# Kernel optimization log

Hardware: AMD Instinct MI355X
Metric: run time of the kernel (lower is better)

Reference implementation:

```python
import jax, jax.numpy as jnp
import numpy as np

H = 4  # attention heads for the single degree-0 fiber

def _layer_norm(x, gamma):
    mu = x.mean(-1, keepdims=True)
    var = ((x - mu) ** 2).mean(-1, keepdims=True)
    return (x - mu) / jnp.sqrt(var + 1e-5) * gamma

def _silu(x):
    return x * jax.nn.sigmoid(x)

def _forward(features, rel_dist, norm_scale, Wq, Wxi, Wxj,
             rp_W1, rp_b1, rp_g1, rp_W2, rp_b2, rp_g2, rp_W3, rp_b3,
             Wkv_out, Wout, neighbor_indices, neighbor_mask):
    b, n, d, _ = features.shape
    k = neighbor_indices.shape[-1]
    hid = Wq.shape[1]
    dh = hid // H
    kvd = Wkv_out.shape[0]
    scale = dh ** -0.5

    # ---- prenorm: RMS (over feature channels) of per-m L2 norms; m=1 for degree 0
    rms = jnp.sqrt(jnp.sum(features ** 2, axis=-2, keepdims=True)) * (d ** -0.5)
    x = features / jnp.maximum(rms, 1e-12) * norm_scale      # (b,n,d,1)
    x = x[..., 0]                                            # (b,n,d)

    # ---- queries
    q = x @ Wq                                               # (b,n,hid)

    # ---- DTP to_kv (degree0->degree0): project xi/xj, gather neighbors, radial kernel
    xi = x @ Wxi
    xj = x @ Wxj
    xg = jax.vmap(lambda t, idx: t[idx])(xj, neighbor_indices)   # (b,n,k,d)
    xe = xg + xi[:, :, None, :]

    hdd = _layer_norm(_silu(rel_dist @ rp_W1 + rp_b1), rp_g1)    # (b,n,k,rh)
    hdd = _layer_norm(_silu(hdd @ rp_W2 + rp_b2), rp_g2)
    R = (hdd @ rp_W3 + rp_b3).reshape(b, n, k, kvd, d)           # per-edge (lo,li) kernel
    kv = jnp.einsum('bnkod,bnkd->bnko', R, xe)                   # (b,n,k,kvd)
    kv = kv @ Wkv_out                                            # DTP project_out
    kk, vv = jnp.split(kv, 2, axis=-1)                           # (b,n,k,hid) each

    # ---- L2-distance attention over neighbors
    qh = q.reshape(b, n, H, dh).transpose(0, 2, 1, 3)            # (b,h,n,dh)
    kh = kk.reshape(b, n, k, H, dh).transpose(0, 3, 1, 2, 4)     # (b,h,n,k,dh)
    vh = vv.reshape(b, n, k, H, dh).transpose(0, 3, 1, 2, 4)
    diff = qh[:, :, :, None, :] - kh + 1e-6                      # F.pairwise_distance eps
    sim = -jnp.sqrt(jnp.sum(diff * diff, axis=-1)) * scale       # (b,h,n,k)
    sim = jnp.where(neighbor_mask[:, None], sim, -jnp.finfo(sim.dtype).max)
    attn = jax.nn.softmax(sim, axis=-1)
    out = jnp.einsum('bhnk,bhnkd->bhnd', attn, vh)
    out = out.transpose(0, 2, 1, 3).reshape(b, n, hid)

    return (out @ Wout)[..., None]                               # (b,n,d,1)

def setup_inputs() -> dict:
    key = jax.random.key(0)
    ks = jax.random.split(key, 16)
    b, n, k, d = 2, 256, 16, 64
    hid = H * 32           # heads * dim_head = 128
    kvd = 2 * hid          # 256
    rh = 64                # radial_hidden_dim
    rnd = lambda i, shape, s=1.0: jax.random.normal(ks[i], shape, jnp.float32) * s
    return dict(
        features=rnd(0, (b, n, d, 1)),
        neighbor_indices=jax.random.randint(ks[1], (b, n, k), 0, n),
        neighbor_mask=jax.random.bernoulli(ks[2], 0.9, (b, n, k)),
        rel_dist=jax.random.uniform(ks[3], (b, n, k, 1), jnp.float32),
        norm_scale=jnp.ones((d, 1), jnp.float32),
        Wq=rnd(4, (d, hid), d ** -0.5),
        Wxi=rnd(5, (d, d), d ** -0.5),
        Wxj=rnd(6, (d, d), d ** -0.5),
        rp_W1=rnd(7, (1, rh)), rp_b1=jnp.zeros((rh,), jnp.float32),
        rp_g1=jnp.ones((rh,), jnp.float32),
        rp_W2=rnd(8, (rh, rh), rh ** -0.5), rp_b2=jnp.zeros((rh,), jnp.float32),
        rp_g2=jnp.ones((rh,), jnp.float32),
        rp_W3=rnd(9, (rh, kvd * d), rh ** -0.5), rp_b3=jnp.zeros((kvd * d,), jnp.float32),
        Wkv_out=rnd(10, (kvd, kvd), kvd ** -0.5),
        Wout=rnd(11, (hid, d), hid ** -0.5),
    )

def reference(features, neighbor_indices, neighbor_mask, rel_dist, norm_scale,
              Wq, Wxi, Wxj, rp_W1, rp_b1, rp_g1, rp_W2, rp_b2, rp_g2,
              rp_W3, rp_b3, Wkv_out, Wout):
    return _forward(features, rel_dist, norm_scale, Wq, Wxi, Wxj,
                    rp_W1, rp_b1, rp_g1, rp_W2, rp_b2, rp_g2, rp_W3, rp_b3,
                    Wkv_out, Wout, neighbor_indices, neighbor_mask)
```

## Files before the change

kernel.cpp:

```cpp
#include <hip/hip_runtime.h>
#include <hip/hip_bf16.h>
#include <float.h>

#define BB 2
#define NN 256
#define DD 64
#define KK 16
#define NH 4
#define HID 128
#define KVD 256
#define RH 64
#define NNODES (BB*NN)
#define NEDGES (NNODES*KK)

typedef unsigned int uint32;
typedef unsigned short ushort_t;
typedef float f32x4_t __attribute__((ext_vector_type(4)));
typedef short bf16x8_t __attribute__((ext_vector_type(8)));
typedef __attribute__((address_space(3))) ushort_t lds_us;
typedef __attribute__((address_space(1))) const ushort_t glb_us;

__device__ __forceinline__ uint32 cvtpk_bf16(float lo, float hi) {
  uint32 r;
  asm("v_cvt_pk_bf16_f32 %0, %1, %2" : "=v"(r) : "v"(lo), "v"(hi));
  return r;
}

__device__ __forceinline__ float wave_sum64(float v) {
  #pragma unroll
  for (int m = 32; m; m >>= 1) v += __shfl_xor(v, m, 64);
  return v;
}

__device__ __forceinline__ ushort_t rne_bf16(float f) {
  uint32 u = __float_as_uint(f);
  return (ushort_t)((u + 0x7FFFu + ((u >> 16) & 1u)) >> 16);
}

__global__ __launch_bounds__(256) void node_w3_kernel(
    const float* __restrict__ feat, const float* __restrict__ gscale,
    const float* __restrict__ Wq, const float* __restrict__ Wxi,
    const float* __restrict__ Wxj,
    const float* __restrict__ W3, const float* __restrict__ b3,
    const float* __restrict__ Wkv,
    float* __restrict__ q_ws, float* __restrict__ xi_ws, float* __restrict__ xj_ws,
    ushort_t* __restrict__ W3bf, ushort_t* __restrict__ Wkvt) {
  int bx = blockIdx.x;
  if (bx >= 648) {
    int i = ((bx - 648) * 256 + threadIdx.x) * 4;
    int n = i >> 8, k0 = i & 255;
    union { uint2 q; ushort_t s[4]; } o;
    #pragma unroll
    for (int j = 0; j < 4; ++j) o.s[j] = rne_bf16(Wkv[(k0 + j) * KVD + n]);
    *(uint2*)(Wkvt + n * KVD + k0) = o.q;
    return;
  }
  if (bx >= 128) {
    const int W3N = 64 * KVD * DD;
    int i = ((bx - 128) * 256 + threadIdx.x) * 8;
    const float* src = (i < W3N) ? (W3 + i) : (b3 + (i - W3N));
    float4 a = ((const float4*)src)[0];
    float4 b = ((const float4*)src)[1];
    float v[8] = {a.x, a.y, a.z, a.w, b.x, b.y, b.z, b.w};
    union { uint4 q; ushort_t s[8]; } o;
    #pragma unroll
    for (int jj = 0; jj < 8; ++jj) o.s[jj] = rne_bf16(v[jj]);
    int rr = i >> 14, j0 = i & 16383;
    int oc = j0 >> 6, gr = (j0 >> 3) & 7;
    int byte_sw = oc * 128 + ((gr * 16) ^ ((oc & 7) << 4));
    *(uint4*)(W3bf + (rr << 14) + (byte_sw >> 1)) = o.q;
    return;
  }
  int sub = threadIdx.x >> 6;
  int t = threadIdx.x & 63;
  int node = bx * 4 + sub;
  __shared__ float xs[4][DD];
  float f = feat[node * DD + t];
  float ss = wave_sum64(f * f);
  float rms = sqrtf(ss) * 0.125f;
  float den = fmaxf(rms, 1e-12f);
  float x = f / den * gscale[t];
  xs[sub][t] = x;
  __syncthreads();
  float q0 = 0.f, q1 = 0.f, xiv = 0.f, xjv = 0.f;
  #pragma unroll 4
  for (int d = 0; d < DD; ++d) {
    float xv = xs[sub][d];
    q0  += xv * Wq[d * HID + t];
    q1  += xv * Wq[d * HID + 64 + t];
    xiv += xv * Wxi[d * DD + t];
    xjv += xv * Wxj[d * DD + t];
  }
  q_ws[node * HID + t] = q0;
  q_ws[node * HID + 64 + t] = q1;
  xi_ws[node * DD + t] = xiv;
  xj_ws[node * DD + t] = xjv;
}

#define AFRAG(dst, arr, base, h) {                                \
  union { bf16x8_t v; uint32 u[4]; } t_;                          \
  t_.u[0] = cvtpk_bf16(arr[(base)+0]*(h), arr[(base)+1]*(h));     \
  t_.u[1] = cvtpk_bf16(arr[(base)+2]*(h), arr[(base)+3]*(h));     \
  t_.u[2] = cvtpk_bf16(arr[(base)+4]*(h), arr[(base)+5]*(h));     \
  t_.u[3] = cvtpk_bf16(arr[(base)+6]*(h), arr[(base)+7]*(h));     \
  dst = t_.v; }

#define STAGE2(buf, rr) {                                                      \
  const ushort_t* s_ = W3bf + ((size_t)(rr) << 14);                            \
  ushort_t* d_ = &bstage[buf][0];                                              \
  __builtin_amdgcn_global_load_lds((glb_us*)(s_ + tid * 8),         (lds_us*)(d_ + tid * 8),         16, 0, 0); \
  __builtin_amdgcn_global_load_lds((glb_us*)(s_ + 2048  + tid * 8), (lds_us*)(d_ + 2048  + tid * 8), 16, 0, 0); \
  __builtin_amdgcn_global_load_lds((glb_us*)(s_ + 4096  + tid * 8), (lds_us*)(d_ + 4096  + tid * 8), 16, 0, 0); \
  __builtin_amdgcn_global_load_lds((glb_us*)(s_ + 6144  + tid * 8), (lds_us*)(d_ + 6144  + tid * 8), 16, 0, 0); \
  __builtin_amdgcn_global_load_lds((glb_us*)(s_ + 8192  + tid * 8), (lds_us*)(d_ + 8192  + tid * 8), 16, 0, 0); \
  __builtin_amdgcn_global_load_lds((glb_us*)(s_ + 10240 + tid * 8), (lds_us*)(d_ + 10240 + tid * 8), 16, 0, 0); \
  __builtin_amdgcn_global_load_lds((glb_us*)(s_ + 12288 + tid * 8), (lds_us*)(d_ + 12288 + tid * 8), 16, 0, 0); \
  __builtin_amdgcn_global_load_lds((glb_us*)(s_ + 14336 + tid * 8), (lds_us*)(d_ + 14336 + tid * 8), 16, 0, 0); }

__global__ __launch_bounds__(256, 1) void fused_kernel(
    const int* __restrict__ nbi, const float* __restrict__ rel,
    const float* __restrict__ W1, const float* __restrict__ b1,
    const float* __restrict__ g1, const float* __restrict__ W2,
    const float* __restrict__ b2, const float* __restrict__ g2,
    const float* __restrict__ xi_ws, const float* __restrict__ xj_ws,
    const ushort_t* __restrict__ W3bf, const ushort_t* __restrict__ Wkvt,
    const float* __restrict__ q_ws, const int* __restrict__ maskp,
    const float* __restrict__ Wout, float* __restrict__ out) {
  int b = blockIdx.x;
  int tid = threadIdx.x;
  int wv = tid >> 6, l = tid & 63;
  int l15 = l & 15, g = l >> 4;

  __shared__ ushort_t bstage[2][16384];
  __shared__ float h2_s[32 * 68];
  __shared__ float xe_s[32 * 68];
  __shared__ float attn_s[2][NH * KK];
  __shared__ float o_s[2][HID];

  STAGE2(0, 0);

  {
    float w1r = W1[l], b1r = b1[l], g1r = g1[l];
    float b2r = b2[l], g2r = g2[l];
    float w2r[64];
    #pragma unroll
    for (int r = 0; r < 64; ++r) w2r[r] = W2[r * RH + l];
    int node_w = b * 2 + (wv >> 1);
    int bbn = node_w >> 8;
    float xir = xi_ws[node_w * DD + l];
    for (int i = 0; i < 8; ++i) {
      int e_loc = wv * 8 + i;
      float rd = rel[b * 32 + e_loc];
      float h = rd * w1r + b1r;
      h = h / (1.f + expf(-h));
      float mu = wave_sum64(h) * (1.f / RH);
      float c = h - mu;
      float var = wave_sum64(c * c) * (1.f / RH);
      float xn = c * rsqrtf(var + 1e-5f) * g1r;
      float p = b2r;
      #pragma unroll
      for (int r = 0; r < 64; ++r) {
        float s = __uint_as_float(__builtin_amdgcn_readlane(__float_as_uint(xn), r));
        p += s * w2r[r];
      }
      p = p / (1.f + expf(-p));
      mu = wave_sum64(p) * (1.f / RH);
      c = p - mu;
      var = wave_sum64(c * c) * (1.f / RH);
      float h2v = c * rsqrtf(var + 1e-5f) * g2r;
      h2_s[e_loc * 68 + l] = h2v;
      int nb = nbi[node_w * KK + (e_loc & 15)];
      xe_s[e_loc * 68 + l] = xj_ws[(bbn * NN + nb) * DD + l] + xir;
    }
  }
  asm volatile("s_waitcnt vmcnt(0)" ::: "memory");
  __syncthreads();

  float xfA[16], xfB[16];
  #pragma unroll
  for (int j = 0; j < 8; ++j) {
    xfA[j]     = xe_s[l15 * 68 + g * 8 + j];
    xfA[8 + j] = xe_s[l15 * 68 + 32 + g * 8 + j];
    xfB[j]     = xe_s[(16 + l15) * 68 + g * 8 + j];
    xfB[8 + j] = xe_s[(16 + l15) * 68 + 32 + g * 8 + j];
  }
  int swz = (l15 & 7) << 4;
  f32x4_t accA[4], accB[4];
  #pragma unroll
  for (int oi = 0; oi < 4; ++oi) {
    accA[oi] = (f32x4_t){0.f, 0.f, 0.f, 0.f};
    accB[oi] = (f32x4_t){0.f, 0.f, 0.f, 0.f};
  }
  int cur = 0;
  for (int p = 0; p <= 64; ++p) {
    if (p < 64) STAGE2(cur ^ 1, p + 1);
    float hA = (p < 64) ? h2_s[l15 * 68 + p] : 1.0f;
    float hB = (p < 64) ? h2_s[(16 + l15) * 68 + p] : 1.0f;
    bf16x8_t a0A, a1A, a0B, a1B;
    AFRAG(a0A, xfA, 0, hA); AFRAG(a1A, xfA, 8, hA);
    AFRAG(a0B, xfB, 0, hB); AFRAG(a1B, xfB, 8, hB);
    const char* bp = (const char*)&bstage[cur][0] + wv * 8192 + l15 * 128;
    #pragma unroll
    for (int oi = 0; oi < 4; ++oi) {
      bf16x8_t bv0 = *(const bf16x8_t*)(bp + oi * 2048 + ((g * 16) ^ swz));
      bf16x8_t bv1 = *(const bf16x8_t*)(bp + oi * 2048 + (((4 + g) * 16) ^ swz));
      accA[oi] = __builtin_amdgcn_mfma_f32_16x16x32_bf16(a0A, bv0, accA[oi], 0, 0, 0);
      accA[oi] = __builtin_amdgcn_mfma_f32_16x16x32_bf16(a1A, bv1, accA[oi], 0, 0, 0);
      accB[oi] = __builtin_amdgcn_mfma_f32_16x16x32_bf16(a0B, bv0, accB[oi], 0, 0, 0);
      accB[oi] = __builtin_amdgcn_mfma_f32_16x16x32_bf16(a1B, bv1, accB[oi], 0, 0, 0);
    }
    asm volatile("s_waitcnt vmcnt(0)" ::: "memory");
    __syncthreads();
    cur ^= 1;
  }

  float* kvf = (float*)&bstage[0][0];
  {
    #pragma unroll
    for (int m = 0; m < 2; ++m) {
      #pragma unroll
      for (int oi = 0; oi < 4; ++oi) {
        f32x4_t av = m ? accB[oi] : accA[oi];
        int f = wv * 64 + oi * 16 + l15;
        int fu = f >> 2, fl = f & 3;
        #pragma unroll
        for (int q = 0; q < 4; ++q) {
          int e = m * 16 + g * 4 + q;
          kvf[e * 256 + ((fu ^ (e & 7)) << 2) + fl] = av[q];
        }
      }
    }
  }
  __syncthreads();

  int role = wv & 1, nl = wv >> 1;
  int node = b * 2 + nl;
  bf16x8_t a[8];
  {
    int e = nl * 16 + l15;
    const float* kr = kvf + e * 256;
    int sw = l15 & 7;
    #pragma unroll
    for (int c = 0; c < 8; ++c) {
      int u0 = (c * 8 + g * 2) ^ sw;
      int u1 = (c * 8 + g * 2 + 1) ^ sw;
      f32x4_t v0 = *(const f32x4_t*)(kr + u0 * 4);
      f32x4_t v1 = *(const f32x4_t*)(kr + u1 * 4);
      union { bf16x8_t v; uint32 u[4]; } t_;
      t_.u[0] = cvtpk_bf16(v0.x, v0.y);
      t_.u[1] = cvtpk_bf16(v0.z, v0.w);
      t_.u[2] = cvtpk_bf16(v1.x, v1.y);
      t_.u[3] = cvtpk_bf16(v1.z, v1.w);
      a[c] = t_.v;
    }
  }
  f32x4_t acc[8];
  #pragma unroll
  for (int nt = 0; nt < 8; ++nt) {
    acc[nt] = (f32x4_t){0.f, 0.f, 0.f, 0.f};
    const ushort_t* bbase = Wkvt + (size_t)(role * 128 + nt * 16 + l15) * KVD + g * 8;
    #pragma unroll
    for (int c = 0; c < 8; ++c) {
      bf16x8_t bv = *(const bf16x8_t*)(bbase + c * 32);
      acc[nt] = __builtin_amdgcn_mfma_f32_16x16x32_bf16(a[c], bv, acc[nt], 0, 0, 0);
    }
  }
  const float scale = 0.17677669529663689f;
  if (role == 0) {
    float sim[4][4];
    #pragma unroll
    for (int h = 0; h < 4; ++h) {
      #pragma unroll
      for (int q = 0; q < 4; ++q) {
        float s = 0.f;
        #pragma unroll
        for (int pq = 0; pq < 2; ++pq) {
          int nt = h * 2 + pq;
          float qv = q_ws[node * HID + nt * 16 + l15];
          float diff = qv - acc[nt][q] + 1e-6f;
          s += diff * diff;
        }
        #pragma unroll
        for (int m = 8; m; m >>= 1) s += __shfl_xor(s, m, 64);
        sim[q][h] = -sqrtf(s) * scale;
      }
    }
    int mv[4];
    #pragma unroll
    for (int q = 0; q < 4; ++q) mv[q] = maskp[node * KK + g * 4 + q];
    #pragma unroll
    for (int h = 0; h < 4; ++h) {
      float sv[4];
      float mx = -FLT_MAX;
      #pragma unroll
      for (int q = 0; q < 4; ++q) {
        sv[q] = mv[q] ? sim[q][h] : -FLT_MAX;
        mx = fmaxf(mx, sv[q]);
      }
      mx = fmaxf(mx, __shfl_xor(mx, 16, 64));
      mx = fmaxf(mx, __shfl_xor(mx, 32, 64));
      float se = 0.f, ev[4];
      #pragma unroll
      for (int q = 0; q < 4; ++q) { ev[q] = expf(sv[q] - mx); se += ev[q]; }
      se += __shfl_xor(se, 16, 64);
      se += __shfl_xor(se, 32, 64);
      float inv = 1.f / se;
      if (l15 == 0) {
        #pragma unroll
        for (int q = 0; q < 4; ++q) attn_s[nl][h * KK + g * 4 + q] = ev[q] * inv;
      }
    }
  }
  __syncthreads();
  if (role == 1) {
    #pragma unroll
    for (int nt = 0; nt < 8; ++nt) {
      int h = nt >> 1;
      float o = 0.f;
      #pragma unroll
      for (int q = 0; q < 4; ++q) o += attn_s[nl][h * KK + g * 4 + q] * acc[nt][q];
      o += __shfl_xor(o, 16, 64);
      o += __shfl_xor(o, 32, 64);
      if (g == 0) o_s[nl][nt * 16 + l15] = o;
    }
  }
  __syncthreads();
  if (tid < 128) {
    int n2 = tid >> 6, t = tid & 63;
    float r = 0.f;
    #pragma unroll 4
    for (int cI = 0; cI < HID; ++cI) r += o_s[n2][cI] * Wout[cI * DD + t];
    out[(b * 2 + n2) * DD + t] = r;
  }
}

extern "C" void kernel_launch(void* const* d_in, const int* in_sizes, int n_in,
                              void* d_out, int out_size, void* d_ws, size_t ws_size,
                              hipStream_t stream) {
  const float* feat = (const float*)d_in[0];
  const int*   nbi  = (const int*)d_in[1];
  const int*   msk  = (const int*)d_in[2];
  const float* rel  = (const float*)d_in[3];
  const float* gsc  = (const float*)d_in[4];
  const float* Wq   = (const float*)d_in[5];
  const float* Wxi  = (const float*)d_in[6];
  const float* Wxj  = (const float*)d_in[7];
  const float* W1   = (const float*)d_in[8];
  const float* b1   = (const float*)d_in[9];
  const float* g1   = (const float*)d_in[10];
  const float* W2   = (const float*)d_in[11];
  const float* b2   = (const float*)d_in[12];
  const float* g2   = (const float*)d_in[13];
  const float* W3   = (const float*)d_in[14];
  const float* b3   = (const float*)d_in[15];
  const float* Wkv  = (const float*)d_in[16];
  const float* Wout = (const float*)d_in[17];

  float* ws      = (float*)d_ws;
  float* q_ws    = ws;
  float* xi_ws   = q_ws  + NNODES * HID;
  float* xj_ws   = xi_ws + NNODES * DD;
  ushort_t* W3bf = (ushort_t*)(xj_ws + NNODES * DD);
  ushort_t* Wkvt = W3bf + 65 * 16384;

  node_w3_kernel<<<712, 256, 0, stream>>>(feat, gsc, Wq, Wxi, Wxj, W3, b3, Wkv,
                                          q_ws, xi_ws, xj_ws, W3bf, Wkvt);
  fused_kernel<<<256, 256, 0, stream>>>(nbi, rel, W1, b1, g1, W2, b2, g2,
                                        xi_ws, xj_ws, W3bf, Wkvt,
                                        q_ws, msk, Wout, (float*)d_out);
}
```

Before: 189.9 us.

## Triple-buffer W3 staging with per-wave loads and drop per-iteration barriers

The W3 weight staging moves from a block-wide double buffer, synchronised by a barrier every iteration, to a triple buffer. Each wave now loads only its own 8 KB slice, so each wave reads only the LDS it fetched itself. The per-iteration s_waitcnt vmcnt(0) plus __syncthreads is replaced with counted vmcnt waits, which lets waves run ahead and keeps up to three stages of loads in flight. This costs an extra 32 KB of LDS and relies on exact vmcnt accounting. It also relies on the hA/hB reads from h2_s and the earlier global loads not disturbing those counts, which is fragile.

```diff
diff --git a/kernel.cpp b/kernel.cpp
--- a/kernel.cpp
+++ b/kernel.cpp
@@ -105,17 +105,17 @@
   t_.u[3] = cvtpk_bf16(arr[(base)+6]*(h), arr[(base)+7]*(h));     \
   dst = t_.v; }
 
-#define STAGE2(buf, rr) {                                                      \
-  const ushort_t* s_ = W3bf + ((size_t)(rr) << 14);                            \
-  ushort_t* d_ = &bstage[buf][0];                                              \
-  __builtin_amdgcn_global_load_lds((glb_us*)(s_ + tid * 8),         (lds_us*)(d_ + tid * 8),         16, 0, 0); \
-  __builtin_amdgcn_global_load_lds((glb_us*)(s_ + 2048  + tid * 8), (lds_us*)(d_ + 2048  + tid * 8), 16, 0, 0); \
-  __builtin_amdgcn_global_load_lds((glb_us*)(s_ + 4096  + tid * 8), (lds_us*)(d_ + 4096  + tid * 8), 16, 0, 0); \
-  __builtin_amdgcn_global_load_lds((glb_us*)(s_ + 6144  + tid * 8), (lds_us*)(d_ + 6144  + tid * 8), 16, 0, 0); \
-  __builtin_amdgcn_global_load_lds((glb_us*)(s_ + 8192  + tid * 8), (lds_us*)(d_ + 8192  + tid * 8), 16, 0, 0); \
-  __builtin_amdgcn_global_load_lds((glb_us*)(s_ + 10240 + tid * 8), (lds_us*)(d_ + 10240 + tid * 8), 16, 0, 0); \
-  __builtin_amdgcn_global_load_lds((glb_us*)(s_ + 12288 + tid * 8), (lds_us*)(d_ + 12288 + tid * 8), 16, 0, 0); \
-  __builtin_amdgcn_global_load_lds((glb_us*)(s_ + 14336 + tid * 8), (lds_us*)(d_ + 14336 + tid * 8), 16, 0, 0); }
+#define STAGEW(slot, rr) {                                                     \
+  const ushort_t* s_ = W3bf + ((size_t)(rr) << 14) + wv * 4096;                \
+  ushort_t* d_ = &bstage[slot][wv * 4096];                                     \
+  __builtin_amdgcn_global_load_lds((glb_us*)(s_ + l * 8),          (lds_us*)(d_ + l * 8),          16, 0, 0); \
+  __builtin_amdgcn_global_load_lds((glb_us*)(s_ + 512  + l * 8),   (lds_us*)(d_ + 512  + l * 8),   16, 0, 0); \
+  __builtin_amdgcn_global_load_lds((glb_us*)(s_ + 1024 + l * 8),   (lds_us*)(d_ + 1024 + l * 8),   16, 0, 0); \
+  __builtin_amdgcn_global_load_lds((glb_us*)(s_ + 1536 + l * 8),   (lds_us*)(d_ + 1536 + l * 8),   16, 0, 0); \
+  __builtin_amdgcn_global_load_lds((glb_us*)(s_ + 2048 + l * 8),   (lds_us*)(d_ + 2048 + l * 8),   16, 0, 0); \
+  __builtin_amdgcn_global_load_lds((glb_us*)(s_ + 2560 + l * 8),   (lds_us*)(d_ + 2560 + l * 8),   16, 0, 0); \
+  __builtin_amdgcn_global_load_lds((glb_us*)(s_ + 3072 + l * 8),   (lds_us*)(d_ + 3072 + l * 8),   16, 0, 0); \
+  __builtin_amdgcn_global_load_lds((glb_us*)(s_ + 3584 + l * 8),   (lds_us*)(d_ + 3584 + l * 8),   16, 0, 0); }
 
 __global__ __launch_bounds__(256, 1) void fused_kernel(
     const int* __restrict__ nbi, const float* __restrict__ rel,
@@ -131,13 +131,15 @@
   int wv = tid >> 6, l = tid & 63;
   int l15 = l & 15, g = l >> 4;
 
-  __shared__ ushort_t bstage[2][16384];
+  __shared__ ushort_t bstage[3][16384];
   __shared__ float h2_s[32 * 68];
   __shared__ float xe_s[32 * 68];
   __shared__ float attn_s[2][NH * KK];
   __shared__ float o_s[2][HID];
 
-  STAGE2(0, 0);
+  STAGEW(0, 0);
+  STAGEW(1, 1);
+  STAGEW(2, 2);
 
   {
     float w1r = W1[l], b1r = b1[l], g1r = g1[l];
@@ -173,7 +175,6 @@
       xe_s[e_loc * 68 + l] = xj_ws[(bbn * NN + nb) * DD + l] + xir;
     }
   }
-  asm volatile("s_waitcnt vmcnt(0)" ::: "memory");
   __syncthreads();
 
   float xfA[16], xfB[16];
@@ -191,15 +192,18 @@
     accA[oi] = (f32x4_t){0.f, 0.f, 0.f, 0.f};
     accB[oi] = (f32x4_t){0.f, 0.f, 0.f, 0.f};
   }
-  int cur = 0;
+  #pragma unroll 1
   for (int p = 0; p <= 64; ++p) {
-    if (p < 64) STAGE2(cur ^ 1, p + 1);
+    if (p < 63)       asm volatile("s_waitcnt vmcnt(16)" ::: "memory");
+    else if (p == 63) asm volatile("s_waitcnt vmcnt(8)"  ::: "memory");
+    else              asm volatile("s_waitcnt vmcnt(0)"  ::: "memory");
+    int slot = p - (p / 3) * 3;
+    const char* bp = (const char*)&bstage[slot][0] + wv * 8192 + l15 * 128;
     float hA = (p < 64) ? h2_s[l15 * 68 + p] : 1.0f;
     float hB = (p < 64) ? h2_s[(16 + l15) * 68 + p] : 1.0f;
     bf16x8_t a0A, a1A, a0B, a1B;
     AFRAG(a0A, xfA, 0, hA); AFRAG(a1A, xfA, 8, hA);
     AFRAG(a0B, xfB, 0, hB); AFRAG(a1B, xfB, 8, hB);
-    const char* bp = (const char*)&bstage[cur][0] + wv * 8192 + l15 * 128;
     #pragma unroll
     for (int oi = 0; oi < 4; ++oi) {
       bf16x8_t bv0 = *(const bf16x8_t*)(bp + oi * 2048 + ((g * 16) ^ swz));
@@ -209,10 +213,9 @@
       accB[oi] = __builtin_amdgcn_mfma_f32_16x16x32_bf16(a0B, bv0, accB[oi], 0, 0, 0);
       accB[oi] = __builtin_amdgcn_mfma_f32_16x16x32_bf16(a1B, bv1, accB[oi], 0, 0, 0);
     }
-    asm volatile("s_waitcnt vmcnt(0)" ::: "memory");
-    __syncthreads();
-    cur ^= 1;
-  }
+    if (p <= 61) STAGEW(slot, p + 3);
+  }
+  __syncthreads();
 
   float* kvf = (float*)&bstage[0][0];
   {
```

Result: faster. 166.5 us (-12.3%).
